# Optimization experiments

Measured on AMD Instinct MI355X. Metric: run time of the kernel, lower is better.

Reference implementation:

```python
import jax, jax.numpy as jnp
import numpy as np

COMMITMENT_COST = 0.25


def setup_inputs() -> dict:
    key = jax.random.key(0)
    k1, k2 = jax.random.split(key)
    inputs = jax.random.normal(k1, (16, 256, 32, 32), dtype=jnp.float32)
    embedding = jax.random.normal(k2, (8192, 256), dtype=jnp.float32)
    return {"inputs": inputs, "embedding": embedding}


def reference(inputs, embedding):
    # inputs: [B, C, H, W] with C == embedding_dim; embedding: [K, C]
    B, C, H, W = inputs.shape
    x = jnp.transpose(inputs, (0, 2, 3, 1))          # [B, H, W, C]
    flat = x.reshape(-1, C)                           # [N, C]
    # squared L2 distances: ||f||^2 + ||e||^2 - 2 f.e
    dist = (jnp.sum(flat * flat, axis=1, keepdims=True)
            + jnp.sum(embedding * embedding, axis=1)
            - 2.0 * flat @ embedding.T)               # [N, K]
    idx = jnp.argmin(dist, axis=1)                    # [N]
    quantized = embedding[idx].reshape(x.shape)       # [B, H, W, C]
    # commitment loss (eval mode: no EMA buffer updates)
    e_latent_loss = jnp.mean((jax.lax.stop_gradient(quantized) - x) ** 2)
    loss = COMMITMENT_COST * e_latent_loss
    # straight-through estimator
    q_st = x + jax.lax.stop_gradient(quantized - x)
    out = jnp.transpose(q_st, (0, 3, 1, 2))           # [B, C, H, W]
    return out, loss, idx.reshape(B, -1)
```

## Files before the change

### kernel.cpp

```cpp
#include <hip/hip_runtime.h>

#define C_   256
#define HW_  1024
#define N_   16384
#define K_   8192
#define OUT_SZ   4194304
#define LOSS_OFF 4194304
#define IDX_OFF  4194305
#define MARGIN   0.3f

typedef __attribute__((ext_vector_type(8)))  short short8;
typedef __attribute__((ext_vector_type(4)))  float f32x4;

#define BH_OFF    0u
#define CNORM_OFF 4194304u
#define LIST_OFF  4227072u
#define CNT_OFF   4292608u
#define FIDX_OFF  4292672u
#define WS_NEED   4358656u

#define FB_CNORM   0u
#define FB_BESTS   32768u
#define FB_BESTK   557056u
#define FB_FIDX    1081344u

__device__ __forceinline__ unsigned short f2bf_rne(float x) {
  unsigned u = __float_as_uint(x);
  unsigned r = (u + 0x7fffu + ((u >> 16) & 1u)) >> 16;
  return (unsigned short)r;
}
__device__ __forceinline__ float bf2f(unsigned short h) {
  return __uint_as_float(((unsigned)h) << 16);
}
__device__ __forceinline__ void gld16(const void* g, void* l) {
  __builtin_amdgcn_global_load_lds((const __attribute__((address_space(1))) unsigned*)g,
                                   (__attribute__((address_space(3))) unsigned*)l, 16, 0, 0);
}

__global__ __launch_bounds__(256) void conv_embn(const float* __restrict__ emb,
                                                 unsigned short* __restrict__ Bh,
                                                 float* __restrict__ cnorm,
                                                 float* __restrict__ loss_slot,
                                                 int* __restrict__ counter) {
  int tid = threadIdx.x, wave = tid >> 6, lane = tid & 63;
  int k = blockIdx.x * 4 + wave;
  float4 v = *(const float4*)(emb + (size_t)k * C_ + lane * 4);
  float ss = v.x*v.x + v.y*v.y + v.z*v.z + v.w*v.w;
  #pragma unroll
  for (int m = 32; m > 0; m >>= 1) ss += __shfl_xor(ss, m);
  if (lane == 0) cnorm[k] = 0.5f * ss;
  uint2 p;
  p.x = (unsigned)f2bf_rne(v.x) | ((unsigned)f2bf_rne(v.y) << 16);
  p.y = (unsigned)f2bf_rne(v.z) | ((unsigned)f2bf_rne(v.w) << 16);
  *(uint2*)&Bh[(size_t)k * C_ + lane * 4] = p;
  if (blockIdx.x == 0 && tid == 0) { *loss_slot = 0.0f; *counter = 0; }
}

__global__ __launch_bounds__(256) void conv_inph(const float* __restrict__ inp,
                                                 unsigned short* __restrict__ Ah) {
  __shared__ float T[64][65];
  int tid = threadIdx.x;
  int nt = blockIdx.x >> 2, ct = blockIdx.x & 3;
  int n0 = nt * 64, c0 = ct * 64;
  int b = n0 >> 10, hw0 = n0 & 1023;
  const float* base = inp + (size_t)b * (C_ * HW_) + hw0;
  #pragma unroll
  for (int i = 0; i < 16; ++i) {
    int cl = i * 4 + (tid >> 6), nl = tid & 63;
    T[nl][cl] = base[(size_t)(c0 + cl) * HW_ + nl];
  }
  __syncthreads();
  #pragma unroll
  for (int i = 0; i < 16; ++i) {
    int nl = i * 4 + (tid >> 6), cl = tid & 63;
    Ah[(size_t)(n0 + nl) * C_ + c0 + cl] = f2bf_rne(T[nl][cl]);
  }
}

__global__ __launch_bounds__(256, 2) void k_gemm1p(const unsigned short* __restrict__ Ah,
                                                   const unsigned short* __restrict__ Bh,
                                                   const float* __restrict__ cnorm,
                                                   uint4* __restrict__ Rec) {
  __shared__ __align__(16) unsigned short LDS[2][12288];
  __shared__ float mS[2][128][3];

  const int tid = threadIdx.x, lane = tid & 63, wave = tid >> 6;
  const int wr = wave >> 1, wc = wave & 1;
  const int rb = blockIdx.x >> 3, kb = blockIdx.x & 7;
  const int row0 = rb * 128;
  const int qm = lane & 15, quad = lane >> 4;
  const int sw = (quad ^ (qm & 3)) * 8;

  const char* srcA[2]; int dstA[2];
  #pragma unroll
  for (int t = 0; t < 2; ++t) {
    int g = t * 256 + tid;
    int row = g >> 2, chs = g & 3, ch = chs ^ (row & 3);
    srcA[t] = (const char*)Ah + (size_t)(row0 + row) * 512 + ch * 16;
    dstA[t] = g * 16;
  }
  const char* srcB[4]; int dstB[4];
  #pragma unroll
  for (int t = 0; t < 4; ++t) {
    int g = t * 256 + tid;
    int r = g >> 2, chs = g & 3, ch = chs ^ (r & 3);
    srcB[t] = (const char*)Bh + (size_t)(kb * 1024 + r) * 512 + ch * 16;
    dstB[t] = 8192 + g * 16;
  }

  #pragma unroll
  for (int t = 0; t < 2; ++t) gld16(srcA[t], (char*)LDS[0] + dstA[t]);
  #pragma unroll
  for (int t = 0; t < 4; ++t) gld16(srcB[t], (char*)LDS[0] + dstB[t]);
  __syncthreads();

  const unsigned wq  = (unsigned)(wc * 128 + quad * 4);
  const unsigned kmk = 0xFFFFFF00u;

  for (int sub = 0; sub < 4; ++sub) {
    const int nbe = kb * 4 + sub;
    f32x4 acc[4][8];
    #pragma unroll
    for (int r = 0; r < 4; ++r)
      #pragma unroll
      for (int c = 0; c < 8; ++c)
        #pragma unroll
        for (int e = 0; e < 4; ++e) acc[r][c][e] = 0.0f;

    #pragma unroll 2
    for (int ci = 0; ci < 8; ++ci) {
      const int it = (sub << 3) | ci;
      const int cur = ci & 1;
      const int nx = it + 1;
      if (nx < 32) {
        const int nsub = nx >> 3, nci = nx & 7, nb = nx & 1;
        #pragma unroll
        for (int t = 0; t < 2; ++t)
          gld16(srcA[t] + nci * 64, (char*)LDS[nb] + dstA[t]);
        #pragma unroll
        for (int t = 0; t < 4; ++t)
          gld16(srcB[t] + nsub * 131072 + nci * 64, (char*)LDS[nb] + dstB[t]);
      }

      const unsigned short* Lb = &LDS[cur][0];
      short8 ah[4];
      #pragma unroll
      for (int rt = 0; rt < 4; ++rt) {
        int row = (wr * 4 + rt) * 16 + qm;
        ah[rt] = *(const short8*)&Lb[row * 32 + sw];
      }
      #pragma unroll
      for (int ch2 = 0; ch2 < 2; ++ch2) {
        short8 bh[4];
        #pragma unroll
        for (int q = 0; q < 4; ++q) {
          int ct = ch2 * 4 + q;
          int r = (wc * 8 + ct) * 16 + qm;
          bh[q] = *(const short8*)&Lb[4096 + r * 32 + sw];
        }
        #pragma unroll
        for (int rt = 0; rt < 4; ++rt)
          #pragma unroll
          for (int q = 0; q < 4; ++q)
            acc[rt][ch2 * 4 + q] =
              __builtin_amdgcn_mfma_f32_16x16x32_bf16(bh[q], ah[rt], acc[rt][ch2 * 4 + q], 0, 0, 0);
      }
      __syncthreads();
    }

    const int cb = nbe * 256 + wc * 128 + quad * 4;
    float4 cn[8];
    #pragma unroll
    for (int ct = 0; ct < 8; ++ct) cn[ct] = *(const float4*)(cnorm + cb + ct * 16);

    #pragma unroll
    for (int rt = 0; rt < 4; ++rt) {
      float t1 = -3.4e38f, t2 = t1, t3 = t1;
      #pragma unroll
      for (int ct = 0; ct < 8; ++ct) {
        float cna[4] = {cn[ct].x, cn[ct].y, cn[ct].z, cn[ct].w};
        #pragma unroll
        for (int rg = 0; rg < 4; ++rg) {
          float s = acc[rt][ct][rg] - cna[rg];
          unsigned idx = wq | (unsigned)(ct * 16 + rg);
          float kf = __uint_as_float((__float_as_uint(s) & kmk) | idx);
          float l1 = fminf(t1, kf); t1 = fmaxf(t1, kf);
          float l2 = fminf(t2, l1); t2 = fmaxf(t2, l1);
          t3 = fmaxf(t3, l2);
        }
      }
      #pragma unroll
      for (int m = 16; m < 64; m <<= 1) {
        float b1 = __shfl_xor(t1, m), b2 = __shfl_xor(t2, m), b3 = __shfl_xor(t3, m);
        float l1 = fminf(t1, b1); t1 = fmaxf(t1, b1);
        float l2 = fminf(t2, l1); t2 = fmaxf(t2, l1);
        t3 = fmaxf(t3, l2);
        float l3 = fminf(t2, b2); t2 = fmaxf(t2, b2);
        t3 = fmaxf(t3, l3);
        t3 = fmaxf(t3, b3);
      }
      if (quad == 0) {
        int rowl = wr * 64 + rt * 16 + qm;
        mS[wc][rowl][0] = t1; mS[wc][rowl][1] = t2; mS[wc][rowl][2] = t3;
      }
    }
    __syncthreads();
    if (tid < 128) {
      float s1 = mS[0][tid][0], s2 = mS[0][tid][1], s3 = mS[0][tid][2];
      float b1 = mS[1][tid][0], b2 = mS[1][tid][1], b3 = mS[1][tid][2];
      float l1 = fminf(s1, b1); s1 = fmaxf(s1, b1);
      float l2 = fminf(s2, l1); s2 = fmaxf(s2, l1);
      s3 = fmaxf(s3, l2);
      float l3 = fminf(s2, b2); s2 = fmaxf(s2, b2);
      s3 = fmaxf(s3, l3);
      s3 = fmaxf(s3, b3);
      unsigned u1 = __float_as_uint(s1), u2 = __float_as_uint(s2), u3 = __float_as_uint(s3);
      uint4 rec;
      rec.x = u1 & kmk;
      rec.y = ((unsigned)f2bf_rne(__uint_as_float(u2 & kmk)) << 16)
            |  (unsigned)f2bf_rne(__uint_as_float(u3 & kmk));
      rec.z = (u1 & 255u) | ((u2 & 255u) << 8) | ((u3 & 255u) << 16);
      rec.w = 0u;
      Rec[(size_t)(row0 + tid) * 32 + nbe] = rec;
    }
  }
}

__global__ __launch_bounds__(256) void k_merge3(const uint4* __restrict__ Rec,
                                                int* __restrict__ fidx,
                                                float* __restrict__ outIdx,
                                                int* __restrict__ list,
                                                int* __restrict__ counter) {
  int row = blockIdx.x * 256 + threadIdx.x;
  const uint4* r = Rec + (size_t)row * 32;
  float g1 = -3.4e38f; int gk = 0;
  #pragma unroll
  for (int s = 0; s < 32; ++s) {
    float s1 = __uint_as_float(r[s].x);
    if (s1 > g1) { g1 = s1; gk = s * 256 + (int)(r[s].z & 255u); }
  }
  float thr = g1 - MARGIN;
  int cnt = 0;
  #pragma unroll
  for (int s = 0; s < 32; ++s) {
    uint4 v = r[s];
    cnt += (__uint_as_float(v.x) >= thr);
    cnt += (bf2f((unsigned short)(v.y >> 16)) >= thr);
    cnt += (bf2f((unsigned short)(v.y & 0xffffu)) >= thr);
  }
  if (cnt == 1) { fidx[row] = gk; outIdx[row] = (float)gk; }
  else { int p = atomicAdd(counter, 1); list[p] = row; }
}

__global__ __launch_bounds__(256) void k_refine(const float* __restrict__ inp,
                                                const float* __restrict__ emb,
                                                const float* __restrict__ cnorm,
                                                const uint4* __restrict__ Rec,
                                                const int* __restrict__ list,
                                                const int* __restrict__ counter,
                                                int* __restrict__ fidx,
                                                float* __restrict__ outIdx) {
  __shared__ float f[256];
  __shared__ float ls1[32];
  __shared__ int   ck[96];
  __shared__ float csc[96];
  __shared__ int   ncand;
  int tid = threadIdx.x, lane = tid & 63, wv = tid >> 6;
  int count = *counter;
  for (int i = blockIdx.x; i < count; i += 4096) {
    int row = list[i];
    __syncthreads();
    f[tid] = inp[(size_t)(row >> 10) * (C_ * HW_) + (size_t)tid * HW_ + (row & 1023)];
    if (tid == 0) ncand = 0;
    if (tid < 32) ls1[tid] = __uint_as_float(Rec[(size_t)row * 32 + tid].x);
    __syncthreads();
    float g1 = ls1[0];
    #pragma unroll
    for (int s = 1; s < 32; ++s) g1 = fmaxf(g1, ls1[s]);
    float thr = g1 - MARGIN;
    if (tid < 32) {
      uint4 v = Rec[(size_t)row * 32 + tid];
      float s1 = __uint_as_float(v.x);
      float s2 = bf2f((unsigned short)(v.y >> 16));
      float s3 = bf2f((unsigned short)(v.y & 0xffffu));
      int b = tid * 256;
      if (s1 >= thr) { int p = atomicAdd(&ncand, 1); ck[p] = b + (int)(v.z & 255u); }
      if (s2 >= thr) { int p = atomicAdd(&ncand, 1); ck[p] = b + (int)((v.z >> 8) & 255u); }
      if (s3 >= thr) { int p = atomicAdd(&ncand, 1); ck[p] = b + (int)((v.z >> 16) & 255u); }
    }
    __syncthreads();
    int nc = ncand;
    for (int c = wv; c < nc; c += 4) {
      int k = ck[c];
      float4 e = ((const float4*)(emb + (size_t)k * C_))[lane];
      float d = f[lane*4]*e.x + f[lane*4+1]*e.y + f[lane*4+2]*e.z + f[lane*4+3]*e.w;
      #pragma unroll
      for (int m = 32; m > 0; m >>= 1) d += __shfl_xor(d, m);
      if (lane == 0) csc[c] = d - cnorm[k];
    }
    __syncthreads();
    if (tid == 0) {
      float bs = csc[0]; int bk = ck[0];
      for (int c = 1; c < nc; ++c)
        if (csc[c] > bs || (csc[c] == bs && ck[c] < bk)) { bs = csc[c]; bk = ck[c]; }
      fidx[row] = bk; outIdx[row] = (float)bk;
    }
    __syncthreads();
  }
}

__global__ __launch_bounds__(256) void k_out(const float* __restrict__ inp,
                                             const float* __restrict__ emb,
                                             const int* __restrict__ fidx,
                                             float* __restrict__ out,
                                             float* __restrict__ loss) {
  __shared__ float Q[32][260];
  int tid = threadIdx.x;
  int n0 = blockIdx.x * 32, b = n0 >> 10, hw0 = n0 & 1023;
  #pragma unroll
  for (int p = 0; p < 8; ++p) {
    int r = p * 4 + (tid >> 6);
    int kq = fidx[n0 + r];
    float4 v = *(const float4*)(emb + (size_t)kq * C_ + (tid & 63) * 4);
    *(float4*)&Q[r][(tid & 63) * 4] = v;
  }
  __syncthreads();
  int hwl = tid & 31, cl = tid >> 5;
  float lsum = 0.0f;
  #pragma unroll
  for (int p = 0; p < 32; ++p) {
    int c = p * 8 + cl;
    size_t a = (size_t)b * (C_ * HW_) + (size_t)c * HW_ + hw0 + hwl;
    float q = Q[hwl][c];
    float x = inp[a];
    out[a] = q;
    float dd = q - x; lsum += dd * dd;
  }
  #pragma unroll
  for (int m = 32; m > 0; m >>= 1) lsum += __shfl_xor(lsum, m);
  __shared__ float red[4];
  if ((tid & 63) == 0) red[tid >> 6] = lsum;
  __syncthreads();
  if (tid == 0)
    atomicAdd(loss, (red[0] + red[1] + red[2] + red[3]) * (0.25f / (float)OUT_SZ));
}

__global__ __launch_bounds__(256) void k_norms_fb(const float* __restrict__ emb,
                                                  float* __restrict__ cnorm,
                                                  float* __restrict__ loss_slot) {
  int tid = threadIdx.x, wave = tid >> 6, lane = tid & 63;
  int k = blockIdx.x * 4 + wave;
  float4 v = *(const float4*)(emb + k * C_ + lane * 4);
  float s = v.x*v.x + v.y*v.y + v.z*v.z + v.w*v.w;
  #pragma unroll
  for (int m = 32; m > 0; m >>= 1) s += __shfl_xor(s, m);
  if (lane == 0) cnorm[k] = 0.5f * s;
  if (blockIdx.x == 0 && tid == 0) *loss_slot = 0.0f;
}

__global__ __launch_bounds__(256) void k_score_fb(const float* __restrict__ inp,
                                                  const float* __restrict__ emb,
                                                  const float* __restrict__ cnorm,
                                                  float* __restrict__ bestS,
                                                  int*   __restrict__ bestK) {
  __shared__ float As[16][132];
  __shared__ float Bs[16][132];
  const int tid = threadIdx.x;
  const int tx = tid & 15, ty = tid >> 4;
  const int rt = blockIdx.x >> 3, ks = blockIdx.x & 7;
  const int row0 = rt * 128;
  const float* Abase = inp + (row0 >> 10) * (C_ * HW_) + (row0 & 1023);
  const int kbase = ks * 1024;
  const int m4  = (tid & 31) << 2;
  const int ccA = tid >> 5;
  const int cc4 = (tid & 3) << 2;
  const int kkB = tid >> 2;

  float rS[8]; int rK[8];
  #pragma unroll
  for (int r = 0; r < 8; ++r) { rS[r] = -3.4e38f; rK[r] = 0; }

  for (int kt = 0; kt < 8; ++kt) {
    const int k0 = kbase + kt * 128;
    float acc[8][8];
    #pragma unroll
    for (int r = 0; r < 8; ++r)
      #pragma unroll
      for (int c = 0; c < 8; ++c) acc[r][c] = 0.f;

    for (int ci = 0; ci < 16; ++ci) {
      const int c0 = ci * 16;
      __syncthreads();
      #pragma unroll
      for (int p = 0; p < 2; ++p) {
        int cc = ccA + p * 8;
        float4 v = *(const float4*)(Abase + (c0 + cc) * HW_ + m4);
        *(float4*)(&As[cc][m4]) = v;
      }
      #pragma unroll
      for (int p = 0; p < 2; ++p) {
        int k = kkB + p * 64;
        float4 v = *(const float4*)(emb + (size_t)(k0 + k) * C_ + c0 + cc4);
        Bs[cc4 + 0][k] = v.x; Bs[cc4 + 1][k] = v.y;
        Bs[cc4 + 2][k] = v.z; Bs[cc4 + 3][k] = v.w;
      }
      __syncthreads();
      #pragma unroll
      for (int cc = 0; cc < 16; ++cc) {
        float4 a0 = *(const float4*)(&As[cc][ty * 8]);
        float4 a1 = *(const float4*)(&As[cc][ty * 8 + 4]);
        float4 b0 = *(const float4*)(&Bs[cc][tx * 8]);
        float4 b1 = *(const float4*)(&Bs[cc][tx * 8 + 4]);
        float a[8] = {a0.x, a0.y, a0.z, a0.w, a1.x, a1.y, a1.z, a1.w};
        float b[8] = {b0.x, b0.y, b0.z, b0.w, b1.x, b1.y, b1.z, b1.w};
        #pragma unroll
        for (int r = 0; r < 8; ++r)
          #pragma unroll
          for (int c = 0; c < 8; ++c) acc[r][c] += a[r] * b[c];
      }
    }
    float cn[8];
    {
      float4 c0v = *(const float4*)(cnorm + k0 + tx * 8);
      float4 c1v = *(const float4*)(cnorm + k0 + tx * 8 + 4);
      cn[0] = c0v.x; cn[1] = c0v.y; cn[2] = c0v.z; cn[3] = c0v.w;
      cn[4] = c1v.x; cn[5] = c1v.y; cn[6] = c1v.z; cn[7] = c1v.w;
    }
    #pragma unroll
    for (int r = 0; r < 8; ++r)
      #pragma unroll
      for (int c = 0; c < 8; ++c) {
        float s = acc[r][c] - cn[c];
        if (s > rS[r]) { rS[r] = s; rK[r] = k0 + tx * 8 + c; }
      }
  }
  #pragma unroll
  for (int r = 0; r < 8; ++r) {
    float s = rS[r]; int kk = rK[r];
    #pragma unroll
    for (int m = 1; m < 16; m <<= 1) {
      float so = __shfl_xor(s, m);
      int   ko = __shfl_xor(kk, m);
      if (so > s || (so == s && ko < kk)) { s = so; kk = ko; }
    }
    if (tx == 0) {
      int row = row0 + ty * 8 + r;
      bestS[ks * N_ + row] = s;
      bestK[ks * N_ + row] = kk;
    }
  }
}

__global__ __launch_bounds__(256) void k_merge_fb(const float* __restrict__ bestS,
                                                  const int*   __restrict__ bestK,
                                                  float* __restrict__ out_idx,
                                                  int*   __restrict__ fidx) {
  int n = blockIdx.x * 256 + threadIdx.x;
  float bs = -3.4e38f; int bk = 0x7fffffff;
  #pragma unroll
  for (int s = 0; s < 8; ++s) {
    float v = bestS[s * N_ + n];
    int  kk = bestK[s * N_ + n];
    if (v > bs || (v == bs && kk < bk)) { bs = v; bk = kk; }
  }
  out_idx[n] = (float)bk;
  fidx[n] = bk;
}

extern "C" void kernel_launch(void* const* d_in, const int* in_sizes, int n_in,
                              void* d_out, int out_size, void* d_ws, size_t ws_size,
                              hipStream_t stream) {
  const float* inp = (const float*)d_in[0];
  const float* emb = (const float*)d_in[1];
  float* out = (float*)d_out;
  char* ws = (char*)d_ws;

  if (ws_size >= (size_t)WS_NEED) {
    unsigned short* Ah = (unsigned short*)d_out;
    uint4* Rec = (uint4*)((char*)d_out + 8388608u);
    unsigned short* Bh = (unsigned short*)(ws + BH_OFF);
    float* cnorm   = (float*)(ws + CNORM_OFF);
    int*   list    = (int*)(ws + LIST_OFF);
    int*   counter = (int*)(ws + CNT_OFF);
    int*   fidx    = (int*)(ws + FIDX_OFF);

    conv_embn <<<K_ / 4, 256, 0, stream>>>(emb, Bh, cnorm, out + LOSS_OFF, counter);
    conv_inph <<<1024,   256, 0, stream>>>(inp, Ah);
    k_gemm1p  <<<1024,   256, 0, stream>>>(Ah, Bh, cnorm, Rec);
    k_merge3  <<<N_/256, 256, 0, stream>>>(Rec, fidx, out + IDX_OFF, list, counter);
    k_refine  <<<4096,   256, 0, stream>>>(inp, emb, cnorm, Rec, list, counter,
                                           fidx, out + IDX_OFF);
    k_out     <<<N_/32,  256, 0, stream>>>(inp, emb, fidx, out, out + LOSS_OFF);
  } else {
    float* cnorm = (float*)(ws + FB_CNORM);
    float* bestS = (float*)(ws + FB_BESTS);
    int*   bestK = (int*)(ws + FB_BESTK);
    int*   fidx  = (int*)(ws + FB_FIDX);

    k_norms_fb <<<K_ / 4, 256, 0, stream>>>(emb, cnorm, out + LOSS_OFF);
    k_score_fb <<<1024,   256, 0, stream>>>(inp, emb, cnorm, bestS, bestK);
    k_merge_fb <<<N_/256, 256, 0, stream>>>(bestS, bestK, out + IDX_OFF, fidx);
    k_out      <<<OUT_SZ/8192, 256, 0, stream>>>(inp, emb, fidx, out, out + LOSS_OFF);
  }
}
```

Baseline: 206.0 us.

## Fuse conversion kernels, preload norms into accumulators, use med3 top-3, transpose Rec layout

Merges the embedding and input bf16 conversion kernels into one launch. The GEMM now seeds its accumulators with negated half-norms instead of subtracting them afterwards, and the top-3 selection uses fmed3. It also replaces the XOR-swizzled LDS layout with a k-chunk-major layout. Rec is stored slot-major so merge and refine reads coalesce, and merge runs with 64-thread blocks. Together these aim to cut launch overhead, epilogue ALU work and strided reads, at the risk of LDS bank conflicts from the unswizzled layout.

```diff
diff --git a/kernel.cpp b/kernel.cpp
--- a/kernel.cpp
+++ b/kernel.cpp
@@ -12,12 +12,13 @@
 typedef __attribute__((ext_vector_type(8)))  short short8;
 typedef __attribute__((ext_vector_type(4)))  float f32x4;
 
-#define BH_OFF    0u
-#define CNORM_OFF 4194304u
-#define LIST_OFF  4227072u
-#define CNT_OFF   4292608u
-#define FIDX_OFF  4292672u
-#define WS_NEED   4358656u
+#define BH_OFF     0u
+#define CNORM_OFF  4194304u
+#define NCNORM_OFF 4227072u
+#define LIST_OFF   4259840u
+#define CNT_OFF    4325376u
+#define FIDX_OFF   4325440u
+#define WS_NEED    4390976u
 
 #define FB_CNORM   0u
 #define FB_BESTS   32768u
@@ -36,50 +37,60 @@
   __builtin_amdgcn_global_load_lds((const __attribute__((address_space(1))) unsigned*)g,
                                    (__attribute__((address_space(3))) unsigned*)l, 16, 0, 0);
 }
-
-__global__ __launch_bounds__(256) void conv_embn(const float* __restrict__ emb,
-                                                 unsigned short* __restrict__ Bh,
-                                                 float* __restrict__ cnorm,
-                                                 float* __restrict__ loss_slot,
-                                                 int* __restrict__ counter) {
-  int tid = threadIdx.x, wave = tid >> 6, lane = tid & 63;
-  int k = blockIdx.x * 4 + wave;
-  float4 v = *(const float4*)(emb + (size_t)k * C_ + lane * 4);
-  float ss = v.x*v.x + v.y*v.y + v.z*v.z + v.w*v.w;
-  #pragma unroll
-  for (int m = 32; m > 0; m >>= 1) ss += __shfl_xor(ss, m);
-  if (lane == 0) cnorm[k] = 0.5f * ss;
-  uint2 p;
-  p.x = (unsigned)f2bf_rne(v.x) | ((unsigned)f2bf_rne(v.y) << 16);
-  p.y = (unsigned)f2bf_rne(v.z) | ((unsigned)f2bf_rne(v.w) << 16);
-  *(uint2*)&Bh[(size_t)k * C_ + lane * 4] = p;
-  if (blockIdx.x == 0 && tid == 0) { *loss_slot = 0.0f; *counter = 0; }
-}
-
-__global__ __launch_bounds__(256) void conv_inph(const float* __restrict__ inp,
-                                                 unsigned short* __restrict__ Ah) {
+__device__ __forceinline__ float med3(float a, float b, float c) {
+#if __has_builtin(__builtin_amdgcn_fmed3f)
+  return __builtin_amdgcn_fmed3f(a, b, c);
+#else
+  return fmaxf(fminf(fmaxf(a, b), c), fminf(a, b));
+#endif
+}
+
+__global__ __launch_bounds__(256) void conv_fused(const float* __restrict__ inp,
+                                                  const float* __restrict__ emb,
+                                                  unsigned short* __restrict__ Ah,
+                                                  unsigned short* __restrict__ Bh,
+                                                  float* __restrict__ cnorm,
+                                                  float* __restrict__ ncnorm,
+                                                  float* __restrict__ loss_slot,
+                                                  int* __restrict__ counter) {
   __shared__ float T[64][65];
   int tid = threadIdx.x;
-  int nt = blockIdx.x >> 2, ct = blockIdx.x & 3;
-  int n0 = nt * 64, c0 = ct * 64;
-  int b = n0 >> 10, hw0 = n0 & 1023;
-  const float* base = inp + (size_t)b * (C_ * HW_) + hw0;
-  #pragma unroll
-  for (int i = 0; i < 16; ++i) {
-    int cl = i * 4 + (tid >> 6), nl = tid & 63;
-    T[nl][cl] = base[(size_t)(c0 + cl) * HW_ + nl];
-  }
-  __syncthreads();
-  #pragma unroll
-  for (int i = 0; i < 16; ++i) {
-    int nl = i * 4 + (tid >> 6), cl = tid & 63;
-    Ah[(size_t)(n0 + nl) * C_ + c0 + cl] = f2bf_rne(T[nl][cl]);
+  if (blockIdx.x < 2048) {
+    int wave = tid >> 6, lane = tid & 63;
+    int k = blockIdx.x * 4 + wave;
+    float4 v = *(const float4*)(emb + (size_t)k * C_ + lane * 4);
+    float ss = v.x*v.x + v.y*v.y + v.z*v.z + v.w*v.w;
+    #pragma unroll
+    for (int m = 32; m > 0; m >>= 1) ss += __shfl_xor(ss, m);
+    if (lane == 0) { cnorm[k] = 0.5f * ss; ncnorm[k] = -0.5f * ss; }
+    uint2 p;
+    p.x = (unsigned)f2bf_rne(v.x) | ((unsigned)f2bf_rne(v.y) << 16);
+    p.y = (unsigned)f2bf_rne(v.z) | ((unsigned)f2bf_rne(v.w) << 16);
+    *(uint2*)&Bh[(size_t)k * C_ + lane * 4] = p;
+    if (blockIdx.x == 0 && tid == 0) { *loss_slot = 0.0f; *counter = 0; }
+  } else {
+    int bb = blockIdx.x - 2048;
+    int nt = bb >> 2, ct = bb & 3;
+    int n0 = nt * 64, c0 = ct * 64;
+    int b = n0 >> 10, hw0 = n0 & 1023;
+    const float* base = inp + (size_t)b * (C_ * HW_) + hw0;
+    #pragma unroll
+    for (int i = 0; i < 16; ++i) {
+      int cl = i * 4 + (tid >> 6), nl = tid & 63;
+      T[nl][cl] = base[(size_t)(c0 + cl) * HW_ + nl];
+    }
+    __syncthreads();
+    #pragma unroll
+    for (int i = 0; i < 16; ++i) {
+      int nl = i * 4 + (tid >> 6), cl = tid & 63;
+      Ah[(size_t)(n0 + nl) * C_ + c0 + cl] = f2bf_rne(T[nl][cl]);
+    }
   }
 }
 
 __global__ __launch_bounds__(256, 2) void k_gemm1p(const unsigned short* __restrict__ Ah,
                                                    const unsigned short* __restrict__ Bh,
-                                                   const float* __restrict__ cnorm,
+                                                   const float* __restrict__ ncnorm,
                                                    uint4* __restrict__ Rec) {
   __shared__ __align__(16) unsigned short LDS[2][12288];
   __shared__ float mS[2][128][3];
@@ -89,22 +100,19 @@
   const int rb = blockIdx.x >> 3, kb = blockIdx.x & 7;
   const int row0 = rb * 128;
   const int qm = lane & 15, quad = lane >> 4;
-  const int sw = (quad ^ (qm & 3)) * 8;
 
   const char* srcA[2]; int dstA[2];
   #pragma unroll
   for (int t = 0; t < 2; ++t) {
     int g = t * 256 + tid;
-    int row = g >> 2, chs = g & 3, ch = chs ^ (row & 3);
-    srcA[t] = (const char*)Ah + (size_t)(row0 + row) * 512 + ch * 16;
+    srcA[t] = (const char*)Ah + (size_t)(row0 + (g & 127)) * 512 + ((g >> 7) & 3) * 16;
     dstA[t] = g * 16;
   }
   const char* srcB[4]; int dstB[4];
   #pragma unroll
   for (int t = 0; t < 4; ++t) {
     int g = t * 256 + tid;
-    int r = g >> 2, chs = g & 3, ch = chs ^ (r & 3);
-    srcB[t] = (const char*)Bh + (size_t)(kb * 1024 + r) * 512 + ch * 16;
+    srcB[t] = (const char*)Bh + (size_t)(kb * 1024 + (g & 255)) * 512 + (g >> 8) * 16;
     dstB[t] = 8192 + g * 16;
   }
 
@@ -114,18 +122,27 @@
   for (int t = 0; t < 4; ++t) gld16(srcB[t], (char*)LDS[0] + dstB[t]);
   __syncthreads();
 
+  const int aBase = quad * 1024 + wr * 512 + qm * 8;
+  const int bBase = 4096 + quad * 2048 + wc * 1024 + qm * 8;
   const unsigned wq  = (unsigned)(wc * 128 + quad * 4);
   const unsigned kmk = 0xFFFFFF00u;
 
   for (int sub = 0; sub < 4; ++sub) {
     const int nbe = kb * 4 + sub;
+    const int cb = nbe * 256 + wc * 128 + quad * 4;
     f32x4 acc[4][8];
-    #pragma unroll
-    for (int r = 0; r < 4; ++r)
-      #pragma unroll
-      for (int c = 0; c < 8; ++c)
-        #pragma unroll
-        for (int e = 0; e < 4; ++e) acc[r][c][e] = 0.0f;
+    {
+      float4 ncn[8];
+      #pragma unroll
+      for (int ct = 0; ct < 8; ++ct) ncn[ct] = *(const float4*)(ncnorm + cb + ct * 16);
+      #pragma unroll
+      for (int r = 0; r < 4; ++r)
+        #pragma unroll
+        for (int c = 0; c < 8; ++c) {
+          acc[r][c][0] = ncn[c].x; acc[r][c][1] = ncn[c].y;
+          acc[r][c][2] = ncn[c].z; acc[r][c][3] = ncn[c].w;
+        }
+    }
 
     #pragma unroll 2
     for (int ci = 0; ci < 8; ++ci) {
@@ -145,19 +162,14 @@
       const unsigned short* Lb = &LDS[cur][0];
       short8 ah[4];
       #pragma unroll
-      for (int rt = 0; rt < 4; ++rt) {
-        int row = (wr * 4 + rt) * 16 + qm;
-        ah[rt] = *(const short8*)&Lb[row * 32 + sw];
-      }
+      for (int rt = 0; rt < 4; ++rt)
+        ah[rt] = *(const short8*)&Lb[aBase + rt * 128];
       #pragma unroll
       for (int ch2 = 0; ch2 < 2; ++ch2) {
         short8 bh[4];
         #pragma unroll
-        for (int q = 0; q < 4; ++q) {
-          int ct = ch2 * 4 + q;
-          int r = (wc * 8 + ct) * 16 + qm;
-          bh[q] = *(const short8*)&Lb[4096 + r * 32 + sw];
-        }
+        for (int q = 0; q < 4; ++q)
+          bh[q] = *(const short8*)&Lb[bBase + (ch2 * 4 + q) * 128];
         #pragma unroll
         for (int rt = 0; rt < 4; ++rt)
           #pragma unroll
@@ -168,35 +180,27 @@
       __syncthreads();
     }
 
-    const int cb = nbe * 256 + wc * 128 + quad * 4;
-    float4 cn[8];
-    #pragma unroll
-    for (int ct = 0; ct < 8; ++ct) cn[ct] = *(const float4*)(cnorm + cb + ct * 16);
-
     #pragma unroll
     for (int rt = 0; rt < 4; ++rt) {
       float t1 = -3.4e38f, t2 = t1, t3 = t1;
       #pragma unroll
-      for (int ct = 0; ct < 8; ++ct) {
-        float cna[4] = {cn[ct].x, cn[ct].y, cn[ct].z, cn[ct].w};
+      for (int ct = 0; ct < 8; ++ct)
         #pragma unroll
         for (int rg = 0; rg < 4; ++rg) {
-          float s = acc[rt][ct][rg] - cna[rg];
-          unsigned idx = wq | (unsigned)(ct * 16 + rg);
-          float kf = __uint_as_float((__float_as_uint(s) & kmk) | idx);
-          float l1 = fminf(t1, kf); t1 = fmaxf(t1, kf);
-          float l2 = fminf(t2, l1); t2 = fmaxf(t2, l1);
-          t3 = fmaxf(t3, l2);
+          unsigned idxv = wq | (unsigned)(ct * 16 + rg);
+          float kf = __uint_as_float((__float_as_uint(acc[rt][ct][rg]) & kmk) | idxv);
+          float n3 = med3(t2, kf, t3);
+          float n2 = med3(t1, kf, t2);
+          t1 = fmaxf(t1, kf);
+          t2 = n2; t3 = n3;
         }
-      }
       #pragma unroll
       for (int m = 16; m < 64; m <<= 1) {
         float b1 = __shfl_xor(t1, m), b2 = __shfl_xor(t2, m), b3 = __shfl_xor(t3, m);
-        float l1 = fminf(t1, b1); t1 = fmaxf(t1, b1);
-        float l2 = fminf(t2, l1); t2 = fmaxf(t2, l1);
-        t3 = fmaxf(t3, l2);
-        float l3 = fminf(t2, b2); t2 = fmaxf(t2, b2);
-        t3 = fmaxf(t3, l3);
+        float n3 = med3(t2, b1, t3);
+        float n2 = med3(t1, b1, t2);
+        t1 = fmaxf(t1, b1); t2 = n2; t3 = n3;
+        n3 = med3(t2, b2, t3); t2 = fmaxf(t2, b2); t3 = n3;
         t3 = fmaxf(t3, b3);
       }
       if (quad == 0) {
@@ -208,11 +212,10 @@
     if (tid < 128) {
       float s1 = mS[0][tid][0], s2 = mS[0][tid][1], s3 = mS[0][tid][2];
       float b1 = mS[1][tid][0], b2 = mS[1][tid][1], b3 = mS[1][tid][2];
-      float l1 = fminf(s1, b1); s1 = fmaxf(s1, b1);
-      float l2 = fminf(s2, l1); s2 = fmaxf(s2, l1);
-      s3 = fmaxf(s3, l2);
-      float l3 = fminf(s2, b2); s2 = fmaxf(s2, b2);
-      s3 = fmaxf(s3, l3);
+      float n3 = med3(s2, b1, s3);
+      float n2 = med3(s1, b1, s2);
+      s1 = fmaxf(s1, b1); s2 = n2; s3 = n3;
+      n3 = med3(s2, b2, s3); s2 = fmaxf(s2, b2); s3 = n3;
       s3 = fmaxf(s3, b3);
       unsigned u1 = __float_as_uint(s1), u2 = __float_as_uint(s2), u3 = __float_as_uint(s3);
       uint4 rec;
@@ -221,29 +224,29 @@
             |  (unsigned)f2bf_rne(__uint_as_float(u3 & kmk));
       rec.z = (u1 & 255u) | ((u2 & 255u) << 8) | ((u3 & 255u) << 16);
       rec.w = 0u;
-      Rec[(size_t)(row0 + tid) * 32 + nbe] = rec;
-    }
-  }
-}
-
-__global__ __launch_bounds__(256) void k_merge3(const uint4* __restrict__ Rec,
-                                                int* __restrict__ fidx,
-                                                float* __restrict__ outIdx,
-                                                int* __restrict__ list,
-                                                int* __restrict__ counter) {
-  int row = blockIdx.x * 256 + threadIdx.x;
-  const uint4* r = Rec + (size_t)row * 32;
+      Rec[(size_t)nbe * N_ + row0 + tid] = rec;
+    }
+  }
+}
+
+__global__ __launch_bounds__(64) void k_merge3(const uint4* __restrict__ Rec,
+                                               int* __restrict__ fidx,
+                                               float* __restrict__ outIdx,
+                                               int* __restrict__ list,
+                                               int* __restrict__ counter) {
+  int row = blockIdx.x * 64 + threadIdx.x;
   float g1 = -3.4e38f; int gk = 0;
   #pragma unroll
   for (int s = 0; s < 32; ++s) {
-    float s1 = __uint_as_float(r[s].x);
-    if (s1 > g1) { g1 = s1; gk = s * 256 + (int)(r[s].z & 255u); }
+    uint4 v = Rec[(size_t)s * N_ + row];
+    float s1 = __uint_as_float(v.x);
+    if (s1 > g1) { g1 = s1; gk = s * 256 + (int)(v.z & 255u); }
   }
   float thr = g1 - MARGIN;
   int cnt = 0;
   #pragma unroll
   for (int s = 0; s < 32; ++s) {
-    uint4 v = r[s];
+    uint4 v = Rec[(size_t)s * N_ + row];
     cnt += (__uint_as_float(v.x) >= thr);
     cnt += (bf2f((unsigned short)(v.y >> 16)) >= thr);
     cnt += (bf2f((unsigned short)(v.y & 0xffffu)) >= thr);
@@ -272,14 +275,14 @@
     __syncthreads();
     f[tid] = inp[(size_t)(row >> 10) * (C_ * HW_) + (size_t)tid * HW_ + (row & 1023)];
     if (tid == 0) ncand = 0;
-    if (tid < 32) ls1[tid] = __uint_as_float(Rec[(size_t)row * 32 + tid].x);
+    if (tid < 32) ls1[tid] = __uint_as_float(Rec[(size_t)tid * N_ + row].x);
     __syncthreads();
     float g1 = ls1[0];
     #pragma unroll
     for (int s = 1; s < 32; ++s) g1 = fmaxf(g1, ls1[s]);
     float thr = g1 - MARGIN;
     if (tid < 32) {
-      uint4 v = Rec[(size_t)row * 32 + tid];
+      uint4 v = Rec[(size_t)tid * N_ + row];
       float s1 = __uint_as_float(v.x);
       float s2 = bf2f((unsigned short)(v.y >> 16));
       float s3 = bf2f((unsigned short)(v.y & 0xffffu));
@@ -480,17 +483,18 @@
     uint4* Rec = (uint4*)((char*)d_out + 8388608u);
     unsigned short* Bh = (unsigned short*)(ws + BH_OFF);
     float* cnorm   = (float*)(ws + CNORM_OFF);
+    float* ncnorm  = (float*)(ws + NCNORM_OFF);
     int*   list    = (int*)(ws + LIST_OFF);
     int*   counter = (int*)(ws + CNT_OFF);
     int*   fidx    = (int*)(ws + FIDX_OFF);
 
-    conv_embn <<<K_ / 4, 256, 0, stream>>>(emb, Bh, cnorm, out + LOSS_OFF, counter);
-    conv_inph <<<1024,   256, 0, stream>>>(inp, Ah);
-    k_gemm1p  <<<1024,   256, 0, stream>>>(Ah, Bh, cnorm, Rec);
-    k_merge3  <<<N_/256, 256, 0, stream>>>(Rec, fidx, out + IDX_OFF, list, counter);
-    k_refine  <<<4096,   256, 0, stream>>>(inp, emb, cnorm, Rec, list, counter,
-                                           fidx, out + IDX_OFF);
-    k_out     <<<N_/32,  256, 0, stream>>>(inp, emb, fidx, out, out + LOSS_OFF);
+    conv_fused <<<3072,   256, 0, stream>>>(inp, emb, Ah, Bh, cnorm, ncnorm,
+                                            out + LOSS_OFF, counter);
+    k_gemm1p   <<<1024,   256, 0, stream>>>(Ah, Bh, ncnorm, Rec);
+    k_merge3   <<<N_/64,  64,  0, stream>>>(Rec, fidx, out + IDX_OFF, list, counter);
+    k_refine   <<<4096,   256, 0, stream>>>(inp, emb, cnorm, Rec, list, counter,
+                                            fidx, out + IDX_OFF);
+    k_out      <<<N_/32,  256, 0, stream>>>(inp, emb, fidx, out, out + LOSS_OFF);
   } else {
     float* cnorm = (float*)(ws + FB_CNORM);
     float* bestS = (float*)(ws + FB_BESTS);
```

New measurement: 233.7 us. 1.13x slower.
